# Optimization experiments

Hardware: AMD Instinct MI355X
Metric: run time of the kernel (lower is better)

## Reference

```python
import jax, jax.numpy as jnp
import numpy as np

EPS = 1e-12  # torch F.normalize eps

def _l2norm(t, axis):
    n = jnp.linalg.norm(t, axis=axis, keepdims=True)
    return t / jnp.maximum(n, EPS)

def setup_inputs() -> dict:
    key = jax.random.key(0)
    ks = jax.random.split(key, 7)
    B, L, D, F, K = 16, 128, 512, 1024, 16
    return {
        "x": jax.random.normal(ks[0], (B, L, D), jnp.float32),
        "W_gate_basis": jax.random.normal(ks[1], (K, D, F), jnp.float32) * (1.0 / np.sqrt(D)),
        "W_up_basis": jax.random.normal(ks[2], (K, D, F), jnp.float32) * (1.0 / np.sqrt(D)),
        "W_down_basis": jax.random.normal(ks[3], (K, F, D), jnp.float32) * (1.0 / np.sqrt(F)),
        "token_coef1": jax.random.normal(ks[4], (L, K), jnp.float32),
        "token_coef2": jax.random.normal(ks[5], (L, K), jnp.float32),
        "token_coef3": jax.random.normal(ks[6], (L, K), jnp.float32),
        "u_scale_param": jnp.ones((1, F), jnp.float32),
        "v_scale_param": jnp.ones((1, F), jnp.float32),
    }

def reference(x, W_gate_basis, W_up_basis, W_down_basis,
              token_coef1, token_coef2, token_coef3,
              u_scale_param, v_scale_param):
    D = x.shape[-1]
    c1 = jax.nn.softmax(token_coef1, axis=-1)
    c2 = jax.nn.softmax(token_coef2, axis=-1)
    c3 = jax.nn.softmax(token_coef3, axis=-1)
    # per-token weights [L, D, F] / [L, F, D]
    W_gate = jnp.einsum('lk,kio->lio', c1, W_gate_basis)
    W_up = jnp.einsum('lk,kio->lio', c2, W_up_basis)
    W_down = jnp.einsum('lk,koj->loj', c3, W_down_basis)
    W_gate = _l2norm(W_gate, axis=1)   # normalize over input dim D
    W_up = _l2norm(W_up, axis=1)
    W_down = _l2norm(W_down, axis=1)   # normalize over hidden dim F
    u = jnp.einsum('bld,ldf->blf', x, W_gate)
    v = jnp.einsum('bld,ldf->blf', x, W_up)
    u_scale = jnp.abs(u_scale_param) * 1.0
    v_scale = jnp.abs(v_scale_param) * jnp.sqrt(jnp.float32(D))
    h = jax.nn.silu(v_scale * v) * (u_scale * u)
    out = jnp.einsum('blf,lfd->bld', h, W_down)
    return _l2norm(out, axis=-1)
```

## Files before the change

kernel.cpp:

```cpp
#include <hip/hip_runtime.h>
#include <hip/hip_bf16.h>
#include <cmath>


typedef _Float16 half8 __attribute__((ext_vector_type(8)));
typedef _Float16 half4 __attribute__((ext_vector_type(4)));
typedef float    f32x4 __attribute__((ext_vector_type(4)));

#define MFMA_F16 __builtin_amdgcn_mfma_f32_16x16x32_f16

static constexpr size_t OFF_P1 = 0;
static constexpr size_t OFF_P2 = 16777216;
static constexpr size_t OFF_P3 = 33554432;
static constexpr size_t OFF_HP = 50331648;
static constexpr size_t WS_FAST = OFF_HP + 4194304;

__global__ __launch_bounds__(256) void prep_basis_all(
    const float* __restrict__ wg, const float* __restrict__ wu,
    const float* __restrict__ wd,
    _Float16* __restrict__ P1, _Float16* __restrict__ P2,
    _Float16* __restrict__ P3)
{
    int z = blockIdx.y;
    const float* src = (z == 0) ? wg : (z == 1) ? wu : wd;
    _Float16*    dst = (z == 0) ? P1 : (z == 1) ? P2 : P3;
    int A  = (z == 2) ? 1024 : 512;
    int Bd = (z == 2) ? 512 : 1024;
    int nb = Bd >> 6;
    int a0 = (blockIdx.x / nb) * 4;
    int b0 = (blockIdx.x % nb) * 64;

    __shared__ __align__(16) float S[16 * 257];
    int tid = threadIdx.x;
#pragma unroll
    for (int k = 0; k < 16; ++k)
        S[k * 257 + tid] =
            src[(size_t)k * A * Bd + (size_t)(a0 + (tid >> 6)) * Bd + b0 + (tid & 63)];
    __syncthreads();

    int a = tid >> 6, b = tid & 63;
    const float* col = &S[tid];
    half8 v0, v1;
#pragma unroll
    for (int k = 0; k < 8; ++k) v0[k] = (_Float16)col[k * 257];
#pragma unroll
    for (int k = 0; k < 8; ++k) v1[k] = (_Float16)col[(k + 8) * 257];
    _Float16* out = dst + ((size_t)(b0 + b) * A + (a0 + a)) * 16;
    *(half8*)out       = v0;
    *(half8*)(out + 8) = v1;
}

__global__ __launch_bounds__(256, 2) void up_fast(
    const _Float16* __restrict__ P1, const _Float16* __restrict__ P2,
    const float* __restrict__ x,
    const float* __restrict__ tc1, const float* __restrict__ tc2,
    const float* __restrict__ usp, const float* __restrict__ vsp,
    _Float16* __restrict__ Hp)
{
    int lg = blockIdx.x >> 6;
    int f0 = (blockIdx.x & 63) * 16;
    int tid = threadIdx.x;
    int w = tid >> 6, lane = tid & 63;
    int n = lane & 15, kc = lane >> 4;

    __shared__ __align__(16) _Float16 Wt[2][16 * 584];
    __shared__ float CN[2 * 256];

    if (tid < 32) {
        int s = tid >> 4, ll = tid & 15;
        const float* row = (s ? tc2 : tc1) + (size_t)(lg * 16 + ll) * 16;
        float e[16], m = -1e30f, sum = 0.f;
#pragma unroll
        for (int k = 0; k < 16; ++k) m = fmaxf(m, row[k]);
#pragma unroll
        for (int k = 0; k < 16; ++k) { e[k] = __expf(row[k] - m); sum += e[k]; }
        float r = 1.f / sum;
#pragma unroll
        for (int k = 0; k < 16; ++k) CN[s * 256 + ll * 16 + k] = e[k] * r;
    }
    __syncthreads();

    half8 cf1 = { 0, 0, 0, 0, 0, 0, 0, 0 };
    half8 cf2 = { 0, 0, 0, 0, 0, 0, 0, 0 };
    if (kc < 2) {
#pragma unroll
        for (int j = 0; j < 8; ++j) {
            cf1[j] = (_Float16)CN[0 * 256 + n * 16 + kc * 8 + j];
            cf2[j] = (_Float16)CN[1 * 256 + n * 16 + kc * 8 + j];
        }
    }

    f32x4 zf = { 0.f, 0.f, 0.f, 0.f };
    f32x4 aU[4], aV[4];
#pragma unroll
    for (int i = 0; i < 4; ++i) { aU[i] = zf; aV[i] = zf; }
    float nsqU[4] = { 0.f, 0.f, 0.f, 0.f };
    float nsqV[4] = { 0.f, 0.f, 0.f, 0.f };
    half8 xf[4];
    half8 pa[2][4][2];

    for (int it = 0; it < 16; ++it) {
        int d0 = it * 32;
#pragma unroll
        for (int m = 0; m < 2; ++m) {
            const _Float16* P = m ? P2 : P1;
#pragma unroll
            for (int fl = 0; fl < 4; ++fl) {
#pragma unroll
                for (int dg = 0; dg < 2; ++dg) {
                    half8 a = { 0, 0, 0, 0, 0, 0, 0, 0 };
                    if (kc < 2)
                        a = *(const half8*)(P +
                            ((size_t)(f0 + w * 4 + fl) * 512 + d0 + dg * 16 + n) * 16 + kc * 8);
                    pa[m][fl][dg] = a;
                }
            }
        }
        if (it > 0) {
#pragma unroll
            for (int li = 0; li < 4; ++li) {
                int l = w * 4 + li;
                half8 wU = *(const half8*)(&Wt[0][l * 584 + n * 36 + kc * 8]);
                half8 wV = *(const half8*)(&Wt[1][l * 584 + n * 36 + kc * 8]);
                aU[li] = MFMA_F16(xf[li], wU, aU[li], 0, 0, 0);
                aV[li] = MFMA_F16(xf[li], wV, aV[li], 0, 0, 0);
            }
        }
#pragma unroll
        for (int li = 0; li < 4; ++li) {
            int l = lg * 16 + w * 4 + li;
            const float* xp = x + ((size_t)n * 128 + l) * 512 + d0 + kc * 8;
            f32x4 v0 = *(const f32x4*)xp;
            f32x4 v1 = *(const f32x4*)(xp + 4);
            half8 h = { (_Float16)v0[0], (_Float16)v0[1], (_Float16)v0[2],
                        (_Float16)v0[3], (_Float16)v1[0], (_Float16)v1[1],
                        (_Float16)v1[2], (_Float16)v1[3] };
            xf[li] = h;
        }
        __syncthreads();
#pragma unroll
        for (int fl = 0; fl < 4; ++fl) {
            int f_l = w * 4 + fl;
#pragma unroll
            for (int dg = 0; dg < 2; ++dg) {
                f32x4 c1 = MFMA_F16(pa[0][fl][dg], cf1, zf, 0, 0, 0);
                nsqU[fl] += c1[0] * c1[0] + c1[1] * c1[1]
                          + c1[2] * c1[2] + c1[3] * c1[3];
                half4 h1 = { (_Float16)c1[0], (_Float16)c1[1],
                             (_Float16)c1[2], (_Float16)c1[3] };
                *(half4*)(&Wt[0][n * 584 + f_l * 36 + dg * 16 + kc * 4]) = h1;
                f32x4 c2 = MFMA_F16(pa[1][fl][dg], cf2, zf, 0, 0, 0);
                nsqV[fl] += c2[0] * c2[0] + c2[1] * c2[1]
                          + c2[2] * c2[2] + c2[3] * c2[3];
                half4 h2 = { (_Float16)c2[0], (_Float16)c2[1],
                             (_Float16)c2[2], (_Float16)c2[3] };
                *(half4*)(&Wt[1][n * 584 + f_l * 36 + dg * 16 + kc * 4]) = h2;
            }
        }
        __syncthreads();
    }
#pragma unroll
    for (int li = 0; li < 4; ++li) {
        int l = w * 4 + li;
        half8 wU = *(const half8*)(&Wt[0][l * 584 + n * 36 + kc * 8]);
        half8 wV = *(const half8*)(&Wt[1][l * 584 + n * 36 + kc * 8]);
        aU[li] = MFMA_F16(xf[li], wU, aU[li], 0, 0, 0);
        aV[li] = MFMA_F16(xf[li], wV, aV[li], 0, 0, 0);
    }

#pragma unroll
    for (int fl = 0; fl < 4; ++fl) {
        float vU = nsqU[fl], vV = nsqV[fl];
        vU += __shfl_xor(vU, 16); vU += __shfl_xor(vU, 32);
        vV += __shfl_xor(vV, 16); vV += __shfl_xor(vV, 32);
        if (kc == 0) {
            CN[0 * 256 + n * 16 + w * 4 + fl] = vU;
            CN[1 * 256 + n * 16 + w * 4 + fl] = vV;
        }
    }
    __syncthreads();

    int f = f0 + n;
    float usv = fabsf(usp[f]);
    float vsv = fabsf(vsp[f]) * 22.627416997969522f;
#pragma unroll
    for (int li = 0; li < 4; ++li) {
        int lgl = lg * 16 + w * 4 + li;
        float r1 = 1.f / fmaxf(sqrtf(CN[0 * 256 + (w * 4 + li) * 16 + n]), 1e-12f);
        float r2 = 1.f / fmaxf(sqrtf(CN[1 * 256 + (w * 4 + li) * 16 + n]), 1e-12f);
#pragma unroll
        for (int i = 0; i < 4; ++i) {
            float u = aU[li][i] * r1;
            float v = aV[li][i] * r2;
            float zz = vsv * v;
            float sil = zz / (1.f + __expf(-zz));
            float h = sil * (usv * u);
            Hp[((size_t)lgl * 16 + kc * 4 + i) * 1024 + f] = (_Float16)h;
        }
    }
}

__global__ __launch_bounds__(256, 2) void down_fast(
    const _Float16* __restrict__ P3, const float* __restrict__ tc3,
    const _Float16* __restrict__ Hp,
    float* __restrict__ Rp, float* __restrict__ Np)
{
    int zh = blockIdx.x >> 8;
    int rem = blockIdx.x & 255;
    int lg = rem >> 5;
    int d0 = (rem & 31) * 16;
    int tid = threadIdx.x;
    int w = tid >> 6, lane = tid & 63;
    int n = lane & 15, kc = lane >> 4;

    __shared__ __align__(16) _Float16 Wt[16 * 584];
    __shared__ float CN[256];

    if (tid < 16) {
        const float* row = tc3 + (size_t)(lg * 16 + tid) * 16;
        float e[16], m = -1e30f, sum = 0.f;
#pragma unroll
        for (int k = 0; k < 16; ++k) m = fmaxf(m, row[k]);
#pragma unroll
        for (int k = 0; k < 16; ++k) { e[k] = __expf(row[k] - m); sum += e[k]; }
        float r = 1.f / sum;
#pragma unroll
        for (int k = 0; k < 16; ++k) CN[tid * 16 + k] = e[k] * r;
    }
    __syncthreads();

    half8 cf3 = { 0, 0, 0, 0, 0, 0, 0, 0 };
    if (kc < 2) {
#pragma unroll
        for (int j = 0; j < 8; ++j)
            cf3[j] = (_Float16)CN[n * 16 + kc * 8 + j];
    }

    f32x4 zf = { 0.f, 0.f, 0.f, 0.f };
    f32x4 aO[4];
#pragma unroll
    for (int i = 0; i < 4; ++i) aO[i] = zf;
    float nsqD[4] = { 0.f, 0.f, 0.f, 0.f };
    half8 hf[4];
    half8 pa[4][2];

    for (int it = 0; it < 8; ++it) {
        int f0 = zh * 256 + it * 32;
#pragma unroll
        for (int dl = 0; dl < 4; ++dl) {
#pragma unroll
            for (int fg = 0; fg < 2; ++fg) {
                half8 a = { 0, 0, 0, 0, 0, 0, 0, 0 };
                if (kc < 2)
                    a = *(const half8*)(P3 +
                        ((size_t)(d0 + w * 4 + dl) * 1024 + f0 + fg * 16 + n) * 16 + kc * 8);
                pa[dl][fg] = a;
            }
        }
        if (it > 0) {
#pragma unroll
            for (int li = 0; li < 4; ++li) {
                int l = w * 4 + li;
                half8 wf = *(const half8*)(&Wt[l * 584 + n * 36 + kc * 8]);
                aO[li] = MFMA_F16(hf[li], wf, aO[li], 0, 0, 0);
            }
        }
#pragma unroll
        for (int li = 0; li < 4; ++li) {
            int l = lg * 16 + w * 4 + li;
            hf[li] = *(const half8*)(Hp + ((size_t)l * 16 + n) * 1024 + f0 + kc * 8);
        }
        __syncthreads();
#pragma unroll
        for (int dl = 0; dl < 4; ++dl) {
            int d_l = w * 4 + dl;
#pragma unroll
            for (int fg = 0; fg < 2; ++fg) {
                f32x4 cw = MFMA_F16(pa[dl][fg], cf3, zf, 0, 0, 0);
                nsqD[dl] += cw[0] * cw[0] + cw[1] * cw[1]
                          + cw[2] * cw[2] + cw[3] * cw[3];
                half4 h4 = { (_Float16)cw[0], (_Float16)cw[1],
                             (_Float16)cw[2], (_Float16)cw[3] };
                *(half4*)(&Wt[n * 584 + d_l * 36 + fg * 16 + kc * 4]) = h4;
            }
        }
        __syncthreads();
    }
#pragma unroll
    for (int li = 0; li < 4; ++li) {
        int l = w * 4 + li;
        half8 wf = *(const half8*)(&Wt[l * 584 + n * 36 + kc * 8]);
        aO[li] = MFMA_F16(hf[li], wf, aO[li], 0, 0, 0);
    }

#pragma unroll
    for (int dl = 0; dl < 4; ++dl) {
        float v = nsqD[dl];
        v += __shfl_xor(v, 16); v += __shfl_xor(v, 32);
        if (kc == 0)
            Np[(size_t)zh * 65536 + (size_t)(lg * 16 + n) * 512 + d0 + w * 4 + dl] = v;
    }
#pragma unroll
    for (int li = 0; li < 4; ++li) {
        int lgl = lg * 16 + w * 4 + li;
#pragma unroll
        for (int i = 0; i < 4; ++i)
            Rp[(size_t)zh * 1048576 +
               ((size_t)(kc * 4 + i) * 128 + lgl) * 512 + d0 + n] = aO[li][i];
    }
}

__global__ __launch_bounds__(128) void final_combine(
    const float* __restrict__ Rp, const float* __restrict__ Np,
    float* __restrict__ out)
{
    int rid = blockIdx.x;
    int l = rid & 127;
    int t = threadIdx.x;
    f32x4 r = { 0.f, 0.f, 0.f, 0.f };
    f32x4 nn = { 0.f, 0.f, 0.f, 0.f };
#pragma unroll
    for (int zh = 0; zh < 4; ++zh) {
        f32x4 rz = *(const f32x4*)(Rp + (size_t)zh * 1048576 + (size_t)rid * 512 + t * 4);
        f32x4 nz = *(const f32x4*)(Np + (size_t)zh * 65536 + (size_t)l * 512 + t * 4);
#pragma unroll
        for (int j = 0; j < 4; ++j) { r[j] += rz[j]; nn[j] += nz[j]; }
    }
    f32x4 y;
#pragma unroll
    for (int j = 0; j < 4; ++j) {
        float rr = 1.f / fmaxf(sqrtf(fmaxf(nn[j], 0.f)), 1e-12f);
        y[j] = r[j] * rr;
    }
    float s = y[0] * y[0] + y[1] * y[1] + y[2] * y[2] + y[3] * y[3];
#pragma unroll
    for (int off = 32; off > 0; off >>= 1) s += __shfl_down(s, off);
    __shared__ float sred[2];
    if ((t & 63) == 0) sred[t >> 6] = s;
    __syncthreads();
    float rr = 1.f / fmaxf(sqrtf(sred[0] + sred[1]), 1e-12f);
    f32x4 o = { y[0] * rr, y[1] * rr, y[2] * rr, y[3] * rr };
    *(f32x4*)(out + (size_t)rid * 512 + t * 4) = o;
}

__global__ __launch_bounds__(256) void up_kernel(
    const float* __restrict__ x,
    const float* __restrict__ wg, const float* __restrict__ wu,
    const float* __restrict__ tc1, const float* __restrict__ tc2,
    const float* __restrict__ usp, const float* __restrict__ vsp,
    _Float16* __restrict__ Hp)
{
    int lg = blockIdx.x >> 6;
    int f0 = (blockIdx.x & 63) * 16;
    int tid = threadIdx.x;
    int w = tid >> 6, lane = tid & 63;
    int n = lane & 15, kc = lane >> 4;

    __shared__ __align__(16) _Float16 Xt[256 * 40];
    __shared__ __align__(16) _Float16 Bh[32 * 16 * 24];
    __shared__ __align__(16) _Float16 Wt[16 * 528];
    __shared__ float CN[2 * 16 * 16];

    if (tid < 32) {
        int s = tid >> 4, ll = tid & 15;
        const float* row = (s ? tc2 : tc1) + (size_t)(lg * 16 + ll) * 16;
        float e[16], m = -1e30f, sum = 0.f;
#pragma unroll
        for (int k = 0; k < 16; ++k) m = fmaxf(m, row[k]);
#pragma unroll
        for (int k = 0; k < 16; ++k) { e[k] = __expf(row[k] - m); sum += e[k]; }
        float r = 1.f / sum;
#pragma unroll
        for (int k = 0; k < 16; ++k) CN[s * 256 + ll * 16 + k] = e[k] * r;
    }
    __syncthreads();

    half8 cf1 = { 0, 0, 0, 0, 0, 0, 0, 0 };
    half8 cf2 = { 0, 0, 0, 0, 0, 0, 0, 0 };
    if (kc < 2) {
#pragma unroll
        for (int j = 0; j < 8; ++j) {
            cf1[j] = (_Float16)CN[0 * 256 + n * 16 + kc * 8 + j];
            cf2[j] = (_Float16)CN[1 * 256 + n * 16 + kc * 8 + j];
        }
    }

    f32x4 zf = { 0.f, 0.f, 0.f, 0.f };
    f32x4 aU[4], aV[4];
#pragma unroll
    for (int i = 0; i < 4; ++i) { aU[i] = zf; aV[i] = zf; }
    float nsqU[4] = { 0.f, 0.f, 0.f, 0.f };
    float nsqV[4] = { 0.f, 0.f, 0.f, 0.f };

    for (int it = 0; it < 16; ++it) {
        int d0 = it * 32;
#pragma unroll
        for (int p = 0; p < 8; ++p) {
            int r = p * 32 + (tid >> 3);
            int fj = tid & 7;
            int ll = r >> 4, b = r & 15;
            f32x4 v = *(const f32x4*)(
                x + ((size_t)(b * 128 + lg * 16 + ll) * 512 + d0 + fj * 4));
            half4 h = { (_Float16)v[0], (_Float16)v[1],
                        (_Float16)v[2], (_Float16)v[3] };
            *(half4*)(&Xt[r * 40 + fj * 4]) = h;
        }
#pragma unroll
        for (int p = 0; p < 8; ++p) {
            int idx = p * 256 + tid;
            int q = idx & 3, dd = (idx >> 2) & 31, k = idx >> 7;
            f32x4 v = *(const f32x4*)(
                wg + ((size_t)k * 512 + d0 + dd) * 1024 + f0 + q * 4);
#pragma unroll
            for (int j = 0; j < 4; ++j)
                Bh[(dd * 16 + q * 4 + j) * 24 + k] = (_Float16)v[j];
        }
        __syncthreads();
#pragma unroll
        for (int fl = 0; fl < 4; ++fl) {
            int f_l = w * 4 + fl;
#pragma unroll
            for (int dg = 0; dg < 2; ++dg) {
                half8 a = { 0, 0, 0, 0, 0, 0, 0, 0 };
                if (kc < 2)
                    a = *(const half8*)(&Bh[((dg * 16 + n) * 16 + f_l) * 24 + kc * 8]);
                f32x4 cw = MFMA_F16(a, cf1, zf, 0, 0, 0);
                nsqU[fl] += cw[0] * cw[0] + cw[1] * cw[1]
                          + cw[2] * cw[2] + cw[3] * cw[3];
                half4 h4 = { (_Float16)cw[0], (_Float16)cw[1],
                             (_Float16)cw[2], (_Float16)cw[3] };
                *(half4*)(&Wt[n * 528 + f_l * 32 + dg * 16 + kc * 4]) = h4;
            }
        }
        __syncthreads();
#pragma unroll
        for (int li = 0; li < 4; ++li) {
            int l = w * 4 + li;
            half8 xf = *(const half8*)(&Xt[(l * 16 + n) * 40 + kc * 8]);
            half8 wf = *(const half8*)(&Wt[l * 528 + n * 32 + kc * 8]);
            aU[li] = MFMA_F16(xf, wf, aU[li], 0, 0, 0);
        }
#pragma unroll
        for (int p = 0; p < 8; ++p) {
            int idx = p * 256 + tid;
            int q = idx & 3, dd = (idx >> 2) & 31, k = idx >> 7;
            f32x4 v = *(const f32x4*)(
                wu + ((size_t)k * 512 + d0 + dd) * 1024 + f0 + q * 4);
#pragma unroll
            for (int j = 0; j < 4; ++j)
                Bh[(dd * 16 + q * 4 + j) * 24 + k] = (_Float16)v[j];
        }
        __syncthreads();
#pragma unroll
        for (int fl = 0; fl < 4; ++fl) {
            int f_l = w * 4 + fl;
#pragma unroll
            for (int dg = 0; dg < 2; ++dg) {
                half8 a = { 0, 0, 0, 0, 0, 0, 0, 0 };
                if (kc < 2)
                    a = *(const half8*)(&Bh[((dg * 16 + n) * 16 + f_l) * 24 + kc * 8]);
                f32x4 cw = MFMA_F16(a, cf2, zf, 0, 0, 0);
                nsqV[fl] += cw[0] * cw[0] + cw[1] * cw[1]
                          + cw[2] * cw[2] + cw[3] * cw[3];
                half4 h4 = { (_Float16)cw[0], (_Float16)cw[1],
                             (_Float16)cw[2], (_Float16)cw[3] };
                *(half4*)(&Wt[n * 528 + f_l * 32 + dg * 16 + kc * 4]) = h4;
            }
        }
        __syncthreads();
#pragma unroll
        for (int li = 0; li < 4; ++li) {
            int l = w * 4 + li;
            half8 xf = *(const half8*)(&Xt[(l * 16 + n) * 40 + kc * 8]);
            half8 wf = *(const half8*)(&Wt[l * 528 + n * 32 + kc * 8]);
            aV[li] = MFMA_F16(xf, wf, aV[li], 0, 0, 0);
        }
        __syncthreads();
    }

#pragma unroll
    for (int fl = 0; fl < 4; ++fl) {
        float vU = nsqU[fl], vV = nsqV[fl];
        vU += __shfl_xor(vU, 16); vU += __shfl_xor(vU, 32);
        vV += __shfl_xor(vV, 16); vV += __shfl_xor(vV, 32);
        if (kc == 0) {
            CN[0 * 256 + n * 16 + w * 4 + fl] = vU;
            CN[1 * 256 + n * 16 + w * 4 + fl] = vV;
        }
    }
    __syncthreads();

    int f = f0 + n;
    float usv = fabsf(usp[f]);
    float vsv = fabsf(vsp[f]) * 22.627416997969522f;
#pragma unroll
    for (int li = 0; li < 4; ++li) {
        int lgl = lg * 16 + w * 4 + li;
        float r1 = 1.f / fmaxf(sqrtf(CN[0 * 256 + (w * 4 + li) * 16 + n]), 1e-12f);
        float r2 = 1.f / fmaxf(sqrtf(CN[1 * 256 + (w * 4 + li) * 16 + n]), 1e-12f);
#pragma unroll
        for (int i = 0; i < 4; ++i) {
            float u = aU[li][i] * r1;
            float v = aV[li][i] * r2;
            float zz = vsv * v;
            float sil = zz / (1.f + __expf(-zz));
            float h = sil * (usv * u);
            Hp[((size_t)lgl * 16 + kc * 4 + i) * 1024 + f] = (_Float16)h;
        }
    }
}

__global__ __launch_bounds__(256) void down_kernel(
    const float* __restrict__ wd, const float* __restrict__ tc3,
    const _Float16* __restrict__ Hp, float* __restrict__ out)
{
    int lg = blockIdx.x >> 5;
    int d0 = (blockIdx.x & 31) * 16;
    int tid = threadIdx.x;
    int w = tid >> 6, lane = tid & 63;
    int n = lane & 15, kc = lane >> 4;

    __shared__ __align__(16) _Float16 Ht[256 * 40];
    __shared__ __align__(16) _Float16 Bh[32 * 16 * 24];
    __shared__ __align__(16) _Float16 Wt[16 * 528];
    __shared__ float CN[16 * 16];

    if (tid < 16) {
        const float* row = tc3 + (size_t)(lg * 16 + tid) * 16;
        float e[16], m = -1e30f, sum = 0.f;
#pragma unroll
        for (int k = 0; k < 16; ++k) m = fmaxf(m, row[k]);
#pragma unroll
        for (int k = 0; k < 16; ++k) { e[k] = __expf(row[k] - m); sum += e[k]; }
        float r = 1.f / sum;
#pragma unroll
        for (int k = 0; k < 16; ++k) CN[tid * 16 + k] = e[k] * r;
    }
    __syncthreads();

    half8 cf3 = { 0, 0, 0, 0, 0, 0, 0, 0 };
    if (kc < 2) {
#pragma unroll
        for (int j = 0; j < 8; ++j)
            cf3[j] = (_Float16)CN[n * 16 + kc * 8 + j];
    }

    f32x4 zf = { 0.f, 0.f, 0.f, 0.f };
    f32x4 aO[4];
#pragma unroll
    for (int i = 0; i < 4; ++i) aO[i] = zf;
    float nsqD[4] = { 0.f, 0.f, 0.f, 0.f };

    for (int it = 0; it < 32; ++it) {
        int f0 = it * 32;
#pragma unroll
        for (int p = 0; p < 8; ++p) {
            int r = p * 32 + (tid >> 3);
            int hj = tid & 7;
            int ll = r >> 4, b = r & 15;
            half4 v = *(const half4*)(
                Hp + ((size_t)(lg * 16 + ll) * 16 + b) * 1024 + f0 + hj * 4);
            *(half4*)(&Ht[r * 40 + hj * 4]) = v;
        }
#pragma unroll
        for (int p = 0; p < 8; ++p) {
            int idx = p * 256 + tid;
            int q = idx & 3, ff = (idx >> 2) & 31, k = idx >> 7;
            f32x4 v = *(const f32x4*)(
                wd + ((size_t)k * 1024 + f0 + ff) * 512 + d0 + q * 4);
#pragma unroll
            for (int j = 0; j < 4; ++j)
                Bh[(ff * 16 + q * 4 + j) * 24 + k] = (_Float16)v[j];
        }
        __syncthreads();
#pragma unroll
        for (int dl = 0; dl < 4; ++dl) {
            int d_l = w * 4 + dl;
#pragma unroll
            for (int fg = 0; fg < 2; ++fg) {
                half8 a = { 0, 0, 0, 0, 0, 0, 0, 0 };
                if (kc < 2)
                    a = *(const half8*)(&Bh[((fg * 16 + n) * 16 + d_l) * 24 + kc * 8]);
                f32x4 cw = MFMA_F16(a, cf3, zf, 0, 0, 0);
                nsqD[dl] += cw[0] * cw[0] + cw[1] * cw[1]
                          + cw[2] * cw[2] + cw[3] * cw[3];
                half4 h4 = { (_Float16)cw[0], (_Float16)cw[1],
                             (_Float16)cw[2], (_Float16)cw[3] };
                *(half4*)(&Wt[n * 528 + d_l * 32 + fg * 16 + kc * 4]) = h4;
            }
        }
        __syncthreads();
#pragma unroll
        for (int li = 0; li < 4; ++li) {
            int l = w * 4 + li;
            half8 hf = *(const half8*)(&Ht[(l * 16 + n) * 40 + kc * 8]);
            half8 wf = *(const half8*)(&Wt[l * 528 + n * 32 + kc * 8]);
            aO[li] = MFMA_F16(hf, wf, aO[li], 0, 0, 0);
        }
        __syncthreads();
    }

#pragma unroll
    for (int dl = 0; dl < 4; ++dl) {
        float v = nsqD[dl];
        v += __shfl_xor(v, 16); v += __shfl_xor(v, 32);
        if (kc == 0) CN[n * 16 + w * 4 + dl] = v;
    }
    __syncthreads();

#pragma unroll
    for (int li = 0; li < 4; ++li) {
        int lgl = lg * 16 + w * 4 + li;
        float r3 = 1.f / fmaxf(sqrtf(CN[(w * 4 + li) * 16 + n]), 1e-12f);
#pragma unroll
        for (int i = 0; i < 4; ++i)
            out[((size_t)(kc * 4 + i) * 128 + lgl) * 512 + d0 + n] = aO[li][i] * r3;
    }
}

__global__ __launch_bounds__(128) void final_kernel(float* __restrict__ out)
{
    int rid = blockIdx.x;
    int t = threadIdx.x;
    f32x4 y = *(const f32x4*)(out + (size_t)rid * 512 + t * 4);
    float s = y[0] * y[0] + y[1] * y[1] + y[2] * y[2] + y[3] * y[3];
#pragma unroll
    for (int off = 32; off > 0; off >>= 1) s += __shfl_down(s, off);
    __shared__ float sred[2];
    if ((t & 63) == 0) sred[t >> 6] = s;
    __syncthreads();
    float rr = 1.f / fmaxf(sqrtf(sred[0] + sred[1]), 1e-12f);
    f32x4 o = { y[0] * rr, y[1] * rr, y[2] * rr, y[3] * rr };
    *(f32x4*)(out + (size_t)rid * 512 + t * 4) = o;
}

extern "C" void kernel_launch(void* const* d_in, const int* in_sizes, int n_in,
                              void* d_out, int out_size, void* d_ws, size_t ws_size,
                              hipStream_t stream)
{
    (void)in_sizes; (void)n_in; (void)out_size;
    const float* x   = (const float*)d_in[0];
    const float* wg  = (const float*)d_in[1];
    const float* wu  = (const float*)d_in[2];
    const float* wd  = (const float*)d_in[3];
    const float* tc1 = (const float*)d_in[4];
    const float* tc2 = (const float*)d_in[5];
    const float* tc3 = (const float*)d_in[6];
    const float* usp = (const float*)d_in[7];
    const float* vsp = (const float*)d_in[8];
    float* outp = (float*)d_out;
    char* ws = (char*)d_ws;

    if (ws_size >= WS_FAST) {
        _Float16* P1 = (_Float16*)(ws + OFF_P1);
        _Float16* P2 = (_Float16*)(ws + OFF_P2);
        _Float16* P3 = (_Float16*)(ws + OFF_P3);
        _Float16* Hp = (_Float16*)(ws + OFF_HP);
        float* Rp = (float*)(ws + OFF_P1);
        float* Np = (float*)(ws + OFF_P2);
        prep_basis_all<<<dim3(2048, 3), dim3(256), 0, stream>>>(wg, wu, wd,
                                                                P1, P2, P3);
        up_fast<<<dim3(512), dim3(256), 0, stream>>>(P1, P2, x, tc1, tc2,
                                                     usp, vsp, Hp);
        down_fast<<<dim3(1024), dim3(256), 0, stream>>>(P3, tc3, Hp, Rp, Np);
        final_combine<<<dim3(2048), dim3(128), 0, stream>>>(Rp, Np, outp);
    } else {
        _Float16* Hp = (_Float16*)ws;
        up_kernel<<<dim3(512), dim3(256), 0, stream>>>(x, wg, wu, tc1, tc2,
                                                       usp, vsp, Hp);
        down_kernel<<<dim3(256), dim3(256), 0, stream>>>(wd, tc3, Hp, outp);
        final_kernel<<<dim3(2048), dim3(128), 0, stream>>>(outp);
    }
}
```

Before: 239.7 us.

## Double-buffer basis loads in up_fast and widen transpose tiles in prep

Result: slower. 331.4 us (+38.2%).

```diff
diff --git a/kernel.cpp b/kernel.cpp
--- a/kernel.cpp
+++ b/kernel.cpp
@@ -24,31 +24,45 @@
     int z = blockIdx.y;
     const float* src = (z == 0) ? wg : (z == 1) ? wu : wd;
     _Float16*    dst = (z == 0) ? P1 : (z == 1) ? P2 : P3;
-    int A  = (z == 2) ? 1024 : 512;
-    int Bd = (z == 2) ? 512 : 1024;
-    int nb = Bd >> 6;
-    int a0 = (blockIdx.x / nb) * 4;
-    int b0 = (blockIdx.x % nb) * 64;
-
-    __shared__ __align__(16) float S[16 * 257];
-    int tid = threadIdx.x;
-#pragma unroll
-    for (int k = 0; k < 16; ++k)
-        S[k * 257 + tid] =
-            src[(size_t)k * A * Bd + (size_t)(a0 + (tid >> 6)) * Bd + b0 + (tid & 63)];
-    __syncthreads();
-
-    int a = tid >> 6, b = tid & 63;
-    const float* col = &S[tid];
-    half8 v0, v1;
-#pragma unroll
-    for (int k = 0; k < 8; ++k) v0[k] = (_Float16)col[k * 257];
-#pragma unroll
-    for (int k = 0; k < 8; ++k) v1[k] = (_Float16)col[(k + 8) * 257];
-    _Float16* out = dst + ((size_t)(b0 + b) * A + (a0 + a)) * 16;
-    *(half8*)out       = v0;
-    *(half8*)(out + 8) = v1;
+    int Amin = (z == 2) ? 1024 : 512;
+    int Bmaj = (z == 2) ? 512 : 1024;
+    int nM = Bmaj >> 4;
+    int m0 = (blockIdx.x / nM) * 32;
+    int M0 = (blockIdx.x % nM) * 16;
+
+    __shared__ float S[16 * 544];
+    int t = threadIdx.x;
+
+    int row = (t >> 2) & 31;
+    int cg  = t & 3;
+    int khi = t >> 7;
+#pragma unroll
+    for (int p = 0; p < 8; ++p) {
+        int k = p * 2 + khi;
+        f32x4 v = *(const f32x4*)(
+            src + (size_t)k * Amin * Bmaj + (size_t)(m0 + row) * Bmaj + M0 + cg * 4);
+#pragma unroll
+        for (int j = 0; j < 4; ++j)
+            S[k * 544 + row * 17 + cg * 4 + j] = v[j];
+    }
+    __syncthreads();
+
+    int mn = t & 31, mjb = t >> 5;
+#pragma unroll
+    for (int q = 0; q < 2; ++q) {
+        int mj = mjb + q * 8;
+        half8 v0, v1;
+#pragma unroll
+        for (int k = 0; k < 8; ++k) v0[k] = (_Float16)S[k * 544 + mn * 17 + mj];
+#pragma unroll
+        for (int k = 0; k < 8; ++k) v1[k] = (_Float16)S[(k + 8) * 544 + mn * 17 + mj];
+        _Float16* out = dst + ((size_t)(M0 + mj) * Amin + m0 + mn) * 16;
+        *(half8*)out       = v0;
+        *(half8*)(out + 8) = v1;
+    }
 }
+
+struct PA { half8 v[2][4][2]; };
 
 __global__ __launch_bounds__(256, 2) void up_fast(
     const _Float16* __restrict__ P1, const _Float16* __restrict__ P2,
@@ -97,35 +111,27 @@
     float nsqU[4] = { 0.f, 0.f, 0.f, 0.f };
     float nsqV[4] = { 0.f, 0.f, 0.f, 0.f };
     half8 xf[4];
-    half8 pa[2][4][2];
-
-    for (int it = 0; it < 16; ++it) {
+    PA paA, paB;
+
+    auto load_pa = [&](int it, PA& dstp) {
         int d0 = it * 32;
 #pragma unroll
         for (int m = 0; m < 2; ++m) {
             const _Float16* P = m ? P2 : P1;
 #pragma unroll
-            for (int fl = 0; fl < 4; ++fl) {
+            for (int fl = 0; fl < 4; ++fl)
 #pragma unroll
                 for (int dg = 0; dg < 2; ++dg) {
                     half8 a = { 0, 0, 0, 0, 0, 0, 0, 0 };
                     if (kc < 2)
                         a = *(const half8*)(P +
                             ((size_t)(f0 + w * 4 + fl) * 512 + d0 + dg * 16 + n) * 16 + kc * 8);
-                    pa[m][fl][dg] = a;
+                    dstp.v[m][fl][dg] = a;
                 }
-            }
-        }
-        if (it > 0) {
-#pragma unroll
-            for (int li = 0; li < 4; ++li) {
-                int l = w * 4 + li;
-                half8 wU = *(const half8*)(&Wt[0][l * 584 + n * 36 + kc * 8]);
-                half8 wV = *(const half8*)(&Wt[1][l * 584 + n * 36 + kc * 8]);
-                aU[li] = MFMA_F16(xf[li], wU, aU[li], 0, 0, 0);
-                aV[li] = MFMA_F16(xf[li], wV, aV[li], 0, 0, 0);
-            }
-        }
+        }
+    };
+    auto load_xf = [&](int it) {
+        int d0 = it * 32;
 #pragma unroll
         for (int li = 0; li < 4; ++li) {
             int l = lg * 16 + w * 4 + li;
@@ -137,19 +143,30 @@
                         (_Float16)v1[2], (_Float16)v1[3] };
             xf[li] = h;
         }
-        __syncthreads();
+    };
+    auto consume = [&]() {
+#pragma unroll
+        for (int li = 0; li < 4; ++li) {
+            int l = w * 4 + li;
+            half8 wU = *(const half8*)(&Wt[0][l * 584 + n * 36 + kc * 8]);
+            half8 wV = *(const half8*)(&Wt[1][l * 584 + n * 36 + kc * 8]);
+            aU[li] = MFMA_F16(xf[li], wU, aU[li], 0, 0, 0);
+            aV[li] = MFMA_F16(xf[li], wV, aV[li], 0, 0, 0);
+        }
+    };
+    auto mix = [&](PA& cur) {
 #pragma unroll
         for (int fl = 0; fl < 4; ++fl) {
             int f_l = w * 4 + fl;
 #pragma unroll
             for (int dg = 0; dg < 2; ++dg) {
-                f32x4 c1 = MFMA_F16(pa[0][fl][dg], cf1, zf, 0, 0, 0);
+                f32x4 c1 = MFMA_F16(cur.v[0][fl][dg], cf1, zf, 0, 0, 0);
                 nsqU[fl] += c1[0] * c1[0] + c1[1] * c1[1]
                           + c1[2] * c1[2] + c1[3] * c1[3];
                 half4 h1 = { (_Float16)c1[0], (_Float16)c1[1],
                              (_Float16)c1[2], (_Float16)c1[3] };
                 *(half4*)(&Wt[0][n * 584 + f_l * 36 + dg * 16 + kc * 4]) = h1;
-                f32x4 c2 = MFMA_F16(pa[1][fl][dg], cf2, zf, 0, 0, 0);
+                f32x4 c2 = MFMA_F16(cur.v[1][fl][dg], cf2, zf, 0, 0, 0);
                 nsqV[fl] += c2[0] * c2[0] + c2[1] * c2[1]
                           + c2[2] * c2[2] + c2[3] * c2[3];
                 half4 h2 = { (_Float16)c2[0], (_Float16)c2[1],
@@ -157,16 +174,30 @@
                 *(half4*)(&Wt[1][n * 584 + f_l * 36 + dg * 16 + kc * 4]) = h2;
             }
         }
-        __syncthreads();
-    }
-#pragma unroll
-    for (int li = 0; li < 4; ++li) {
-        int l = w * 4 + li;
-        half8 wU = *(const half8*)(&Wt[0][l * 584 + n * 36 + kc * 8]);
-        half8 wV = *(const half8*)(&Wt[1][l * 584 + n * 36 + kc * 8]);
-        aU[li] = MFMA_F16(xf[li], wU, aU[li], 0, 0, 0);
-        aV[li] = MFMA_F16(xf[li], wV, aV[li], 0, 0, 0);
-    }
+    };
+
+    load_pa(0, paA);
+    for (int j = 0; j < 8; ++j) {
+        {
+            int it = 2 * j;
+            if (it < 15) load_pa(it + 1, paB);
+            if (it > 0) consume();
+            load_xf(it);
+            __syncthreads();
+            mix(paA);
+            __syncthreads();
+        }
+        {
+            int it = 2 * j + 1;
+            if (it < 15) load_pa(it + 1, paA);
+            consume();
+            load_xf(it);
+            __syncthreads();
+            mix(paB);
+            __syncthreads();
+        }
+    }
+    consume();
 
 #pragma unroll
     for (int fl = 0; fl < 4; ++fl) {
@@ -658,7 +689,7 @@
         _Float16* Hp = (_Float16*)(ws + OFF_HP);
         float* Rp = (float*)(ws + OFF_P1);
         float* Np = (float*)(ws + OFF_P2);
-        prep_basis_all<<<dim3(2048, 3), dim3(256), 0, stream>>>(wg, wu, wd,
+        prep_basis_all<<<dim3(1024, 3), dim3(256), 0, stream>>>(wg, wu, wd,
                                                                 P1, P2, P3);
         up_fast<<<dim3(512), dim3(256), 0, stream>>>(P1, P2, x, tc1, tc2,
                                                      usp, vsp, Hp);
```
